# Performance work log

Measured on AMD Instinct MI355X. Metric: run time of the kernel, lower is better.

Reference implementation:

```python
import jax, jax.numpy as jnp
import numpy as np

B, S, D = 4, 8192, 1024
H = 16
HD = D // H          # 64
AD = 64              # approx_dim
EPS = 1e-6


def setup_inputs() -> dict:
    key = jax.random.key(0)
    ks = jax.random.split(key, 5)
    x = jax.random.normal(ks[0], (B, S, D), dtype=jnp.float32)
    # qkv_proj: Linear(D, 3*D)
    W_qkv = jax.random.normal(ks[1], (3 * D, D), dtype=jnp.float32) * (1.0 / np.sqrt(D))
    b_qkv = jnp.zeros((3 * D,), dtype=jnp.float32)
    # proj: Linear(HD, AD) with xavier_uniform init, zero bias
    limit = np.sqrt(6.0 / (HD + AD))
    W_p = jax.random.uniform(ks[2], (AD, HD), dtype=jnp.float32, minval=-limit, maxval=limit)
    b_p = jnp.zeros((AD,), dtype=jnp.float32)
    return {"x": x, "W_qkv": W_qkv, "b_qkv": b_qkv, "W_p": W_p, "b_p": b_p}


def reference(x, W_qkv, b_qkv, W_p, b_p):
    # qkv projection and split
    qkv = x @ W_qkv.T + b_qkv                      # [B,S,3D]
    Q, K, V = jnp.split(qkv, 3, axis=-1)
    # [B,S,D] -> [B,H,S,HD]
    def to_heads(t):
        return t.reshape(B, S, H, HD).transpose(0, 2, 1, 3)
    Q, K, V = to_heads(Q), to_heads(K), to_heads(V)
    # shared projection to approx dim, feature map phi(u) = sqrt(1 + u^2)
    pQ = jnp.einsum('bhsd,ad->bhsa', Q, W_p) + b_p
    pK = jnp.einsum('bhsd,ad->bhsa', K, W_p) + b_p
    phi_Q = jnp.sqrt(1.0 + pQ * pQ)                # [B,H,S,AD]
    phi_K = jnp.sqrt(1.0 + pK * pK)
    # linear attention: O(S) chained contractions
    KTV = jnp.einsum('bhsa,bhsv->bhav', phi_K, V)  # [B,H,AD,HD]
    numerator = jnp.einsum('bhsa,bhav->bhsv', phi_Q, KTV)  # [B,H,S,HD]
    k_sum = phi_K.sum(axis=2)                      # [B,H,AD]
    denominator = jnp.einsum('bhsa,bha->bhs', phi_Q, k_sum)  # [B,H,S]
    head_out = numerator / (denominator[..., None] + EPS)
    # [B,H,S,HD] -> [B,S,D]
    return head_out.transpose(0, 2, 1, 3).reshape(B, S, D)
```

## Files before the change

### kernel.cpp

```cpp
#include <hip/hip_runtime.h>
#include <hip/hip_bf16.h>
#include <cstdint>

static constexpr int Bc  = 4;
static constexpr int Sc  = 8192;
static constexpr int Dc  = 1024;
static constexpr int Hc  = 16;
static constexpr int BHc = Bc * Hc;
static constexpr int Mc  = Bc * Sc;
static constexpr int N3c = 3 * Dc;
static constexpr float EPSc = 1e-6f;

using bf16x8 = __attribute__((ext_vector_type(8))) __bf16;
using f32x4  = __attribute__((ext_vector_type(4))) float;

__device__ __forceinline__ ushort f2bf(float f) {
  union { float f; uint32_t u; } v; v.f = f;
  uint32_t u = v.u;
  return (ushort)((u + 0x7fffu + ((u >> 16) & 1u)) >> 16);
}
__device__ __forceinline__ float bf2f(ushort h) {
  union { uint32_t u; float f; } v; v.u = ((uint32_t)h) << 16;
  return v.f;
}

typedef const __attribute__((address_space(1))) unsigned int* gas_u32p;
typedef __attribute__((address_space(3))) unsigned int* las_u32p;
__device__ __forceinline__ void gld_lds16(const void* g, void* l) {
  __builtin_amdgcn_global_load_lds((gas_u32p)g, (las_u32p)l, 16, 0, 0);
}

__global__ __launch_bounds__(256) void cvt_bf16_k(const float* __restrict__ src,
                                                  ushort* __restrict__ dst, int n4) {
  for (int i = blockIdx.x * 256 + threadIdx.x; i < n4; i += gridDim.x * 256) {
    float4 v = reinterpret_cast<const float4*>(src)[i];
    ushort4 o; o.x = f2bf(v.x); o.y = f2bf(v.y); o.z = f2bf(v.z); o.w = f2bf(v.w);
    reinterpret_cast<ushort4*>(dst)[i] = o;
  }
}

__global__ __launch_bounds__(256) void fold_k(const float* __restrict__ Wq,
                                              const float* __restrict__ Wp,
                                              const float* __restrict__ bq,
                                              const float* __restrict__ bp,
                                              ushort* __restrict__ W3b,
                                              float* __restrict__ bias3) {
  const int bx = blockIdx.x;
  const int p = bx >> 4, h = bx & 15;
  const int t = threadIdx.x;
  if (p == 2) {
    const int base = 2048 + h * 64;
    for (int li = t; li < 64 * 256; li += 256) {
      int r = li >> 8, c4 = (li & 255) * 4;
      float4 v = *reinterpret_cast<const float4*>(&Wq[(size_t)(base + r) * 1024 + c4]);
      ushort4 o; o.x = f2bf(v.x); o.y = f2bf(v.y); o.z = f2bf(v.z); o.w = f2bf(v.w);
      *reinterpret_cast<ushort4*>(&W3b[(size_t)(base + r) * 1024 + c4]) = o;
    }
    if (t < 64) bias3[base + t] = bq[base + t];
    return;
  }
  __shared__ ushort Ws[64 * 64];
  __shared__ ushort Tq[256 * 64];
  const int rbase = p * 1024 + h * 64;
  for (int li = t; li < 64 * 16; li += 256) {
    int a = li >> 4, h4 = (li & 15) * 4;
    float4 v = *reinterpret_cast<const float4*>(&Wp[a * 64 + h4]);
    ushort4 o; o.x = f2bf(v.x); o.y = f2bf(v.y); o.z = f2bf(v.z); o.w = f2bf(v.w);
    *reinterpret_cast<ushort4*>(&Ws[a * 64 + h4]) = o;
  }
  if (t < 64) {
    float s = bp[t];
    for (int hd = 0; hd < 64; ++hd) s += Wp[t * 64 + hd] * bq[rbase + hd];
    bias3[rbase + t] = s;
  }
  const int w = t >> 6, lane = t & 63, lr = lane & 15, kg = lane >> 4;
  for (int dt = 0; dt < 4; ++dt) {
    __syncthreads();
    for (int li = t; li < 64 * 64; li += 256) {
      int hd = li >> 6, d4 = (li & 63) * 4;
      float4 v = *reinterpret_cast<const float4*>(&Wq[(size_t)(rbase + hd) * 1024 + dt * 256 + d4]);
      Tq[(d4 + 0) * 64 + hd] = f2bf(v.x);
      Tq[(d4 + 1) * 64 + hd] = f2bf(v.y);
      Tq[(d4 + 2) * 64 + hd] = f2bf(v.z);
      Tq[(d4 + 3) * 64 + hd] = f2bf(v.w);
    }
    __syncthreads();
    f32x4 acc[4][4];
#pragma unroll
    for (int i = 0; i < 4; i++)
#pragma unroll
      for (int j = 0; j < 4; j++) acc[i][j] = (f32x4){0.f, 0.f, 0.f, 0.f};
#pragma unroll
    for (int kk = 0; kk < 2; ++kk) {
      bf16x8 af[4], bfr[4];
#pragma unroll
      for (int i = 0; i < 4; i++)
        af[i] = *reinterpret_cast<const bf16x8*>(&Ws[(i * 16 + lr) * 64 + kk * 32 + kg * 8]);
#pragma unroll
      for (int j = 0; j < 4; j++)
        bfr[j] = *reinterpret_cast<const bf16x8*>(&Tq[(w * 64 + j * 16 + lr) * 64 + kk * 32 + kg * 8]);
#pragma unroll
      for (int i = 0; i < 4; i++)
#pragma unroll
        for (int j = 0; j < 4; j++)
          acc[i][j] = __builtin_amdgcn_mfma_f32_16x16x32_bf16(af[i], bfr[j], acc[i][j], 0, 0, 0);
    }
#pragma unroll
    for (int i = 0; i < 4; i++)
#pragma unroll
      for (int j = 0; j < 4; j++)
#pragma unroll
        for (int r = 0; r < 4; r++)
          W3b[(size_t)(rbase + i * 16 + kg * 4 + r) * 1024 + dt * 256 + w * 64 + j * 16 + lr] =
              f2bf(acc[i][j][r]);
  }
}

__global__ __launch_bounds__(512, 2) void gemm_pipe_k(const ushort* __restrict__ xb,
                                                      const ushort* __restrict__ W3b,
                                                      const float* __restrict__ bias3,
                                                      ushort* __restrict__ Qb,
                                                      ushort* __restrict__ KTb,
                                                      ushort* __restrict__ VTb) {
  __shared__ __align__(16) ushort As[4 * 8192];
  __shared__ __align__(16) ushort Bs[4 * 8192];
  const int t = threadIdx.x, wave = t >> 6, lane = t & 63;
  const int lr = lane & 15, kg = lane >> 4;
  const int wr = wave >> 2, wc = wave & 3;

  const int flat = blockIdx.x;
  const int swz  = (flat & 7) * 192 + (flat >> 3);
  const int n0 = (swz % 12) * 256;
  const int m0 = (swz / 12) * 256;

  const int srow = t >> 2;
  const int sg   = (t & 3) ^ ((t >> 3) & 3);
  const int swb  = wave * 512;

  auto STAGE = [&](int tile, int buf) {
    const int kt = tile * 32;
#pragma unroll
    for (int is = 0; is < 2; ++is) {
      gld_lds16(xb  + (size_t)(m0 + is * 128 + srow) * 1024 + kt + sg * 8,
                As + buf * 8192 + is * 4096 + swb);
      gld_lds16(W3b + (size_t)(n0 + is * 128 + srow) * 1024 + kt + sg * 8,
                Bs + buf * 8192 + is * 4096 + swb);
    }
  };

  f32x4 acc[8][4];
#pragma unroll
  for (int f = 0; f < 8; f++)
#pragma unroll
    for (int j = 0; j < 4; j++) acc[f][j] = (f32x4){0.f, 0.f, 0.f, 0.f};

  const int cp = (kg ^ ((lr >> 1) & 3)) * 8;
  const ushort* Ard = As + (wr * 128 + lr) * 32 + cp;
  const ushort* Brd = Bs + (wc * 64 + lr) * 32 + cp;

  auto COMPUTE = [&](int buf) {
    bf16x8 af[8], bfr[4];
    const ushort* Ab = Ard + buf * 8192;
    const ushort* Bb = Brd + buf * 8192;
#pragma unroll
    for (int f = 0; f < 8; f++) af[f] = *reinterpret_cast<const bf16x8*>(Ab + f * 512);
#pragma unroll
    for (int j = 0; j < 4; j++) bfr[j] = *reinterpret_cast<const bf16x8*>(Bb + j * 512);
    __builtin_amdgcn_s_setprio(1);
#pragma unroll
    for (int f = 0; f < 8; f++)
#pragma unroll
      for (int j = 0; j < 4; j++)
        acc[f][j] = __builtin_amdgcn_mfma_f32_16x16x32_bf16(af[f], bfr[j], acc[f][j], 0, 0, 0);
    __builtin_amdgcn_s_setprio(0);
  };

  STAGE(0, 0);
  STAGE(1, 1);
  STAGE(2, 2);
  asm volatile("s_waitcnt vmcnt(8)" ::: "memory");
  __builtin_amdgcn_s_barrier();

#pragma unroll 1
  for (int i = 0; i < 7; ++i) {
    const int tb = i * 4;
#pragma unroll
    for (int j = 0; j < 4; ++j) {
      STAGE(tb + j + 3, (j + 3) & 3);
      COMPUTE(j);
      asm volatile("s_waitcnt vmcnt(8)" ::: "memory");
      __builtin_amdgcn_s_barrier();
    }
  }
  STAGE(31, 3);
  COMPUTE(0);
  asm volatile("s_waitcnt vmcnt(8)" ::: "memory");
  __builtin_amdgcn_s_barrier();
  COMPUTE(1);
  asm volatile("s_waitcnt vmcnt(4)" ::: "memory");
  __builtin_amdgcn_s_barrier();
  COMPUTE(2);
  asm volatile("s_waitcnt vmcnt(0)" ::: "memory");
  __builtin_amdgcn_s_barrier();
  COMPUTE(3);

  const int n0w  = n0 + wc * 64;
  const int part = n0w >> 10;
  const int h    = (n0w & 1023) >> 6;
  const int bq   = m0 >> 13;
  const int s_base = (m0 & 8191) + wr * 128;
  float bias[4];
#pragma unroll
  for (int j = 0; j < 4; j++) bias[j] = bias3[n0w + j * 16 + lr];

  if (part == 0) {
    ushort* dst = Qb + ((size_t)(bq * Hc + h)) * Sc * 64;
#pragma unroll
    for (int f = 0; f < 8; f++)
#pragma unroll
      for (int j = 0; j < 4; j++)
#pragma unroll
        for (int r = 0; r < 4; r++) {
          float p = acc[f][j][r] + bias[j];
          dst[(size_t)(s_base + f * 16 + kg * 4 + r) * 64 + j * 16 + lr] =
              f2bf(sqrtf(1.f + p * p));
        }
  } else {
    ushort* dst = ((part == 1) ? KTb : VTb) + ((size_t)(bq * Hc + h)) * 64 * Sc;
#pragma unroll
    for (int f = 0; f < 8; f++) {
      const int s = s_base + f * 16 + kg * 4;
#pragma unroll
      for (int j = 0; j < 4; j++) {
        ushort4 o;
        if (part == 1) {
#pragma unroll
          for (int r = 0; r < 4; r++) {
            float p = acc[f][j][r] + bias[j];
            (&o.x)[r] = f2bf(sqrtf(1.f + p * p));
          }
        } else {
#pragma unroll
          for (int r = 0; r < 4; r++) (&o.x)[r] = f2bf(acc[f][j][r] + bias[j]);
        }
        *reinterpret_cast<ushort4*>(&dst[(size_t)(j * 16 + lr) * Sc + s]) = o;
      }
    }
  }
}

__global__ __launch_bounds__(256) void ktv_part_k(const ushort* __restrict__ KT,
                                                  const ushort* __restrict__ VT,
                                                  float* __restrict__ KTVp,
                                                  float* __restrict__ ksump) {
  __shared__ __align__(16) ushort Ks[64 * 128];
  __shared__ __align__(16) ushort Vs[64 * 128];
  __shared__ float red[64][65];
  const int t = threadIdx.x, chunk = blockIdx.x, bh = blockIdx.y;
  const int wave = t >> 6, lane = t & 63, lr = lane & 15, kg = lane >> 4;
  const size_t hb = (size_t)bh * 64 * Sc;
  const int s0 = chunk * 1024;

  f32x4 acc[4][4];
#pragma unroll
  for (int i = 0; i < 4; i++)
#pragma unroll
    for (int j = 0; j < 4; j++) acc[i][j] = (f32x4){0.f, 0.f, 0.f, 0.f};
  float ks_acc = 0.f;

  const int srl = t >> 4;
  const int scc = (t & 15) ^ ((t >> 4) & 7);
  const int wb  = (t >> 6) * 512;
  const int cR = ((wave * 4 + kg) ^ (lr & 7)) * 8;

  for (int st = 0; st < 8; ++st) {
    const int sb = s0 + st * 128;
    __syncthreads();
#pragma unroll
    for (int is = 0; is < 4; ++is) {
      const int row = is * 16 + srl;
      gld_lds16(KT + hb + (size_t)row * Sc + sb + scc * 8, Ks + is * 2048 + wb);
      gld_lds16(VT + hb + (size_t)row * Sc + sb + scc * 8, Vs + is * 2048 + wb);
    }
    __syncthreads();
    {
      bf16x8 af[4], bfr[4];
#pragma unroll
      for (int i = 0; i < 4; i++)
        af[i] = *reinterpret_cast<const bf16x8*>(&Ks[(i * 16 + lr) * 128 + cR]);
#pragma unroll
      for (int j = 0; j < 4; j++)
        bfr[j] = *reinterpret_cast<const bf16x8*>(&Vs[(j * 16 + lr) * 128 + cR]);
#pragma unroll
      for (int i = 0; i < 4; i++)
#pragma unroll
        for (int j = 0; j < 4; j++)
          acc[i][j] = __builtin_amdgcn_mfma_f32_16x16x32_bf16(af[i], bfr[j], acc[i][j], 0, 0, 0);
    }
    if (t < 64) {
      float s = 0.f;
      for (int e = 0; e < 128; e++) s += bf2f(Ks[t * 128 + e]);
      ks_acc += s;
    }
  }

  __syncthreads();
  for (int li = t; li < 64 * 65; li += 256) (&red[0][0])[li] = 0.f;
  __syncthreads();
  for (int w = 0; w < 4; w++) {
    if (wave == w) {
#pragma unroll
      for (int i = 0; i < 4; i++)
#pragma unroll
        for (int j = 0; j < 4; j++)
#pragma unroll
          for (int r = 0; r < 4; r++)
            red[i * 16 + kg * 4 + r][j * 16 + lr] += acc[i][j][r];
    }
    __syncthreads();
  }
  float* outp = KTVp + ((size_t)bh * 8 + chunk) * 4096;
  for (int li = t; li < 4096; li += 256) outp[li] = red[li >> 6][li & 63];
  if (t < 64) ksump[((size_t)bh * 8 + chunk) * 64 + t] = ks_acc;
}

__global__ __launch_bounds__(256) void ktv_red_k(const float* __restrict__ KTVp,
                                                 const float* __restrict__ ksump,
                                                 float* __restrict__ KTV,
                                                 float* __restrict__ ksum) {
  const int bh = blockIdx.x, t = threadIdx.x;
  for (int li = t; li < 4096; li += 256) {
    float s = 0.f;
    for (int c = 0; c < 8; c++) s += KTVp[((size_t)bh * 8 + c) * 4096 + li];
    KTV[(size_t)bh * 4096 + li] = s;
  }
  if (t < 64) {
    float s = 0.f;
    for (int c = 0; c < 8; c++) s += ksump[((size_t)bh * 8 + c) * 64 + t];
    ksum[bh * 64 + t] = s;
  }
}

__global__ __launch_bounds__(256) void out_k(const ushort* __restrict__ Qphi,
                                             const float* __restrict__ KTV,
                                             const float* __restrict__ ksum,
                                             float* __restrict__ out) {
  __shared__ ushort Qs[256][72];
  __shared__ ushort BT[64][72];
  __shared__ float  den[256];
  __shared__ float  kss[64];
  const int t = threadIdx.x;
  const int bh = blockIdx.y, s0 = blockIdx.x * 256;
  const ushort* qb = Qphi + (size_t)bh * Sc * 64 + (size_t)s0 * 64;

#pragma unroll
  for (int i = 0; i < 8; i++) {
    int li = i * 256 + t;
    int r = li >> 3, c8 = li & 7;
    *reinterpret_cast<uint4*>(&Qs[r][c8 * 8]) = *reinterpret_cast<const uint4*>(&qb[li * 8]);
  }
  for (int li = t; li < 4096; li += 256) {
    int a = li >> 6, v = li & 63;
    BT[v][a] = f2bf(KTV[(size_t)bh * 4096 + li]);
  }
  if (t < 64) kss[t] = ksum[bh * 64 + t];
  __syncthreads();

  {
    float d = 0.f;
    for (int a = 0; a < 64; a++) d += bf2f(Qs[t][a]) * kss[a];
    den[t] = d + EPSc;
  }
  __syncthreads();

  const int wave = t >> 6, lane = t & 63, lr = lane & 15, kg = lane >> 4;
  f32x4 acc[4][4];
#pragma unroll
  for (int i = 0; i < 4; i++)
#pragma unroll
    for (int j = 0; j < 4; j++) acc[i][j] = (f32x4){0.f, 0.f, 0.f, 0.f};

#pragma unroll
  for (int ks = 0; ks < 64; ks += 32) {
    bf16x8 af[4], bfr[4];
#pragma unroll
    for (int i = 0; i < 4; i++)
      af[i] = *reinterpret_cast<const bf16x8*>(&Qs[wave * 64 + i * 16 + lr][ks + kg * 8]);
#pragma unroll
    for (int j = 0; j < 4; j++)
      bfr[j] = *reinterpret_cast<const bf16x8*>(&BT[j * 16 + lr][ks + kg * 8]);
#pragma unroll
    for (int i = 0; i < 4; i++)
#pragma unroll
      for (int j = 0; j < 4; j++)
        acc[i][j] = __builtin_amdgcn_mfma_f32_16x16x32_bf16(af[i], bfr[j], acc[i][j], 0, 0, 0);
  }

  const int bq = bh >> 4, h = bh & 15;
#pragma unroll
  for (int i = 0; i < 4; i++) {
#pragma unroll
    for (int j = 0; j < 4; j++) {
#pragma unroll
      for (int r = 0; r < 4; r++) {
        int row = wave * 64 + i * 16 + kg * 4 + r;
        int s = s0 + row;
        int v = j * 16 + lr;
        out[((size_t)bq * Sc + s) * 1024 + h * 64 + v] = acc[i][j][r] / den[row];
      }
    }
  }
}

extern "C" void kernel_launch(void* const* d_in, const int* in_sizes, int n_in,
                              void* d_out, int out_size, void* d_ws, size_t ws_size,
                              hipStream_t stream) {
  const float* x     = (const float*)d_in[0];
  const float* W_qkv = (const float*)d_in[1];
  const float* b_qkv = (const float*)d_in[2];
  const float* W_p   = (const float*)d_in[3];
  const float* b_p   = (const float*)d_in[4];
  float* out = (float*)d_out;

  size_t off = 0;
  auto carve = [&](size_t bytes) -> void* {
    void* p = (char*)d_ws + off;
    off += (bytes + 255) & ~(size_t)255;
    return p;
  };
  const size_t headElems = (size_t)BHc * Sc * 64;
  ushort* xb    = (ushort*)carve((size_t)Mc * Dc * 2);
  ushort* Qb    = (ushort*)carve(headElems * 2);
  ushort* KTb   = (ushort*)carve(headElems * 2);
  ushort* VTb   = (ushort*)carve(headElems * 2);
  ushort* W3b   = (ushort*)carve((size_t)N3c * Dc * 2);
  float*  bias3 = (float*)carve((size_t)N3c * 4);
  float*  KTVp  = (float*)carve((size_t)BHc * 8 * 4096 * 4);
  float*  ksmp  = (float*)carve((size_t)BHc * 8 * 64 * 4);
  float*  KTV   = (float*)carve((size_t)BHc * 4096 * 4);
  float*  ksum  = (float*)carve((size_t)BHc * 64 * 4);
  (void)ws_size; (void)n_in; (void)in_sizes; (void)out_size;

  cvt_bf16_k<<<2048, 256, 0, stream>>>(x, xb, Mc * Dc / 4);
  fold_k<<<48, 256, 0, stream>>>(W_qkv, W_p, b_qkv, b_p, W3b, bias3);
  gemm_pipe_k<<<(Mc / 256) * (N3c / 256), 512, 0, stream>>>(xb, W3b, bias3, Qb, KTb, VTb);
  ktv_part_k<<<dim3(8, BHc), 256, 0, stream>>>(KTb, VTb, KTVp, ksmp);
  ktv_red_k<<<BHc, 256, 0, stream>>>(KTVp, ksmp, KTV, ksum);
  out_k<<<dim3(Sc / 256, BHc), 256, 0, stream>>>(Qb, KTV, ksum, out);
}
```

Before: 417.5 us.

## Restructure QKV GEMM mainloop into 64-wide K double buffer with interleaved staging

Result: slower. 441.1 us (+5.7%).

```diff
diff --git a/kernel.cpp b/kernel.cpp
--- a/kernel.cpp
+++ b/kernel.cpp
@@ -29,6 +29,9 @@
 __device__ __forceinline__ void gld_lds16(const void* g, void* l) {
   __builtin_amdgcn_global_load_lds((gas_u32p)g, (las_u32p)l, 16, 0, 0);
 }
+
+#define FENCE asm volatile("" ::: "memory")
+#define BARF  do { FENCE; __builtin_amdgcn_s_barrier(); FENCE; } while (0)
 
 __global__ __launch_bounds__(256) void cvt_bf16_k(const float* __restrict__ src,
                                                   ushort* __restrict__ dst, int n4) {
@@ -122,8 +125,8 @@
                                                       ushort* __restrict__ Qb,
                                                       ushort* __restrict__ KTb,
                                                       ushort* __restrict__ VTb) {
-  __shared__ __align__(16) ushort As[4 * 8192];
-  __shared__ __align__(16) ushort Bs[4 * 8192];
+  __shared__ __align__(16) ushort As[2 * 16384];
+  __shared__ __align__(16) ushort Bs[2 * 16384];
   const int t = threadIdx.x, wave = t >> 6, lane = t & 63;
   const int lr = lane & 15, kg = lane >> 4;
   const int wr = wave >> 2, wc = wave & 3;
@@ -133,19 +136,23 @@
   const int n0 = (swz % 12) * 256;
   const int m0 = (swz / 12) * 256;
 
-  const int srow = t >> 2;
-  const int sg   = (t & 3) ^ ((t >> 3) & 3);
-  const int swb  = wave * 512;
-
-  auto STAGE = [&](int tile, int buf) {
-    const int kt = tile * 32;
-#pragma unroll
-    for (int is = 0; is < 2; ++is) {
-      gld_lds16(xb  + (size_t)(m0 + is * 128 + srow) * 1024 + kt + sg * 8,
-                As + buf * 8192 + is * 4096 + swb);
-      gld_lds16(W3b + (size_t)(n0 + is * 128 + srow) * 1024 + kt + sg * 8,
-                Bs + buf * 8192 + is * 4096 + swb);
-    }
+  const int srow8 = wave * 8 + (lane >> 3);
+  const int sg    = (lane & 7) ^ (lane >> 3);
+  const int swb   = wave * 512;
+
+  auto stageA = [&](int tile, int buf, int h) {
+    const int col = tile * 64 + sg * 8;
+#pragma unroll
+    for (int i2 = 0; i2 < 2; ++i2)
+      gld_lds16(xb + (size_t)(m0 + h * 128 + i2 * 64 + srow8) * 1024 + col,
+                As + buf * 16384 + h * 8192 + i2 * 4096 + swb);
+  };
+  auto stageB = [&](int tile, int buf, int h) {
+    const int col = tile * 64 + sg * 8;
+#pragma unroll
+    for (int i2 = 0; i2 < 2; ++i2)
+      gld_lds16(W3b + (size_t)(n0 + h * 128 + i2 * 64 + srow8) * 1024 + col,
+                Bs + buf * 16384 + h * 8192 + i2 * 4096 + swb);
   };
 
   f32x4 acc[8][4];
@@ -154,55 +161,72 @@
 #pragma unroll
     for (int j = 0; j < 4; j++) acc[f][j] = (f32x4){0.f, 0.f, 0.f, 0.f};
 
-  const int cp = (kg ^ ((lr >> 1) & 3)) * 8;
-  const ushort* Ard = As + (wr * 128 + lr) * 32 + cp;
-  const ushort* Brd = Bs + (wc * 64 + lr) * 32 + cp;
-
-  auto COMPUTE = [&](int buf) {
-    bf16x8 af[8], bfr[4];
-    const ushort* Ab = Ard + buf * 8192;
-    const ushort* Bb = Brd + buf * 8192;
-#pragma unroll
-    for (int f = 0; f < 8; f++) af[f] = *reinterpret_cast<const bf16x8*>(Ab + f * 512);
-#pragma unroll
-    for (int j = 0; j < 4; j++) bfr[j] = *reinterpret_cast<const bf16x8*>(Bb + j * 512);
+  auto readA4 = [&](int buf, int fh, int kk, bf16x8* a) {
+#pragma unroll
+    for (int f = 0; f < 4; f++) {
+      const int row = wr * 128 + fh * 64 + f * 16 + lr;
+      const int gp  = (kk * 4 + kg) ^ (lr & 7);
+      a[f] = *reinterpret_cast<const bf16x8*>(As + buf * 16384 + row * 64 + gp * 8);
+    }
+  };
+  auto readB4 = [&](int buf, int kk, bf16x8* b) {
+#pragma unroll
+    for (int j = 0; j < 4; j++) {
+      const int row = wc * 64 + j * 16 + lr;
+      const int gp  = (kk * 4 + kg) ^ (lr & 7);
+      b[j] = *reinterpret_cast<const bf16x8*>(Bs + buf * 16384 + row * 64 + gp * 8);
+    }
+  };
+  auto mfma16 = [&](const bf16x8* a, const bf16x8* b, int fh) {
     __builtin_amdgcn_s_setprio(1);
 #pragma unroll
-    for (int f = 0; f < 8; f++)
-#pragma unroll
-      for (int j = 0; j < 4; j++)
-        acc[f][j] = __builtin_amdgcn_mfma_f32_16x16x32_bf16(af[f], bfr[j], acc[f][j], 0, 0, 0);
+    for (int f = 0; f < 4; f++)
+#pragma unroll
+      for (int j = 0; j < 4; j++)
+        acc[fh * 4 + f][j] =
+            __builtin_amdgcn_mfma_f32_16x16x32_bf16(a[f], b[j], acc[fh * 4 + f][j], 0, 0, 0);
     __builtin_amdgcn_s_setprio(0);
   };
 
-  STAGE(0, 0);
-  STAGE(1, 1);
-  STAGE(2, 2);
-  asm volatile("s_waitcnt vmcnt(8)" ::: "memory");
-  __builtin_amdgcn_s_barrier();
+  stageB(0, 0, 0); stageB(0, 0, 1);
+  stageA(0, 0, 0); stageA(0, 0, 1);
+  stageB(1, 1, 0); stageB(1, 1, 1);
+  asm volatile("s_waitcnt vmcnt(4)" ::: "memory");
+  BARF;
+
+  bf16x8 a[4], b[4];
+  auto TILE = [&](int T, int buf, bool stA, bool stB, int W) {
+    if (stA) stageA(T + 1, buf ^ 1, 0);
+    readB4(buf, 0, b);
+    readA4(buf, 0, 0, a);
+    BARF;
+    mfma16(a, b, 0);
+    BARF;
+    if (stA) stageA(T + 1, buf ^ 1, 1);
+    readA4(buf, 1, 0, a);
+    BARF;
+    mfma16(a, b, 1);
+    BARF;
+    readB4(buf, 1, b);
+    readA4(buf, 0, 1, a);
+    BARF;
+    mfma16(a, b, 0);
+    BARF;
+    if (stB) { stageB(T + 2, buf, 0); stageB(T + 2, buf, 1); }
+    readA4(buf, 1, 1, a);
+    BARF;
+    mfma16(a, b, 1);
+    if (W == 4) asm volatile("s_waitcnt vmcnt(4)" ::: "memory");
+    else        asm volatile("s_waitcnt vmcnt(0)" ::: "memory");
+    BARF;
+  };
 
 #pragma unroll 1
-  for (int i = 0; i < 7; ++i) {
-    const int tb = i * 4;
-#pragma unroll
-    for (int j = 0; j < 4; ++j) {
-      STAGE(tb + j + 3, (j + 3) & 3);
-      COMPUTE(j);
-      asm volatile("s_waitcnt vmcnt(8)" ::: "memory");
-      __builtin_amdgcn_s_barrier();
-    }
-  }
-  STAGE(31, 3);
-  COMPUTE(0);
-  asm volatile("s_waitcnt vmcnt(8)" ::: "memory");
-  __builtin_amdgcn_s_barrier();
-  COMPUTE(1);
-  asm volatile("s_waitcnt vmcnt(4)" ::: "memory");
-  __builtin_amdgcn_s_barrier();
-  COMPUTE(2);
-  asm volatile("s_waitcnt vmcnt(0)" ::: "memory");
-  __builtin_amdgcn_s_barrier();
-  COMPUTE(3);
+  for (int tt = 0; tt < 8; ++tt) {
+    const int T0 = tt * 2, T1 = T0 + 1;
+    TILE(T0, 0, true,     T0 < 14, (T0 <= 13) ? 4 : 0);
+    TILE(T1, 1, T1 < 15,  T1 < 14, (T1 <= 13) ? 4 : 0);
+  }
 
   const int n0w  = n0 + wc * 64;
   const int part = n0w >> 10;
```

## Load B operand directly from global into registers, dropping its LDS staging

Applied to the files above, without the earlier changes.

Result: slower. 495.2 us (+18.6%).

```diff
diff --git a/kernel.cpp b/kernel.cpp
--- a/kernel.cpp
+++ b/kernel.cpp
@@ -123,29 +123,32 @@
                                                       ushort* __restrict__ KTb,
                                                       ushort* __restrict__ VTb) {
   __shared__ __align__(16) ushort As[4 * 8192];
-  __shared__ __align__(16) ushort Bs[4 * 8192];
   const int t = threadIdx.x, wave = t >> 6, lane = t & 63;
   const int lr = lane & 15, kg = lane >> 4;
   const int wr = wave >> 2, wc = wave & 3;
 
   const int flat = blockIdx.x;
-  const int swz  = (flat & 7) * 192 + (flat >> 3);
-  const int n0 = (swz % 12) * 256;
-  const int m0 = (swz / 12) * 256;
+  const int xcd = flat & 7, idx = flat >> 3;
+  const int m0 = ((xcd >> 1) * 32 + idx / 6) * 256;
+  const int n0 = ((xcd & 1) * 6 + idx % 6) * 256;
 
   const int srow = t >> 2;
   const int sg   = (t & 3) ^ ((t >> 3) & 3);
   const int swb  = wave * 512;
 
-  auto STAGE = [&](int tile, int buf) {
-    const int kt = tile * 32;
-#pragma unroll
-    for (int is = 0; is < 2; ++is) {
-      gld_lds16(xb  + (size_t)(m0 + is * 128 + srow) * 1024 + kt + sg * 8,
+  auto stageA = [&](int tile, int buf) {
+#pragma unroll
+    for (int is = 0; is < 2; ++is)
+      gld_lds16(xb + (size_t)(m0 + is * 128 + srow) * 1024 + tile * 32 + sg * 8,
                 As + buf * 8192 + is * 4096 + swb);
-      gld_lds16(W3b + (size_t)(n0 + is * 128 + srow) * 1024 + kt + sg * 8,
-                Bs + buf * 8192 + is * 4096 + swb);
-    }
+  };
+
+  const int n0w = n0 + wc * 64;
+  auto loadB = [&](int tile, bf16x8 (&bb)[4]) {
+#pragma unroll
+    for (int j = 0; j < 4; ++j)
+      bb[j] = *reinterpret_cast<const bf16x8*>(
+          W3b + (size_t)(n0w + j * 16 + lr) * 1024 + tile * 32 + kg * 8);
   };
 
   f32x4 acc[8][4];
@@ -156,55 +159,71 @@
 
   const int cp = (kg ^ ((lr >> 1) & 3)) * 8;
   const ushort* Ard = As + (wr * 128 + lr) * 32 + cp;
-  const ushort* Brd = Bs + (wc * 64 + lr) * 32 + cp;
-
-  auto COMPUTE = [&](int buf) {
-    bf16x8 af[8], bfr[4];
+
+  auto compute = [&](int buf, const bf16x8 (&bb)[4]) {
     const ushort* Ab = Ard + buf * 8192;
-    const ushort* Bb = Brd + buf * 8192;
-#pragma unroll
-    for (int f = 0; f < 8; f++) af[f] = *reinterpret_cast<const bf16x8*>(Ab + f * 512);
-#pragma unroll
-    for (int j = 0; j < 4; j++) bfr[j] = *reinterpret_cast<const bf16x8*>(Bb + j * 512);
+    bf16x8 a[4];
+#pragma unroll
+    for (int f = 0; f < 4; ++f) a[f] = *reinterpret_cast<const bf16x8*>(Ab + f * 512);
     __builtin_amdgcn_s_setprio(1);
 #pragma unroll
-    for (int f = 0; f < 8; f++)
-#pragma unroll
-      for (int j = 0; j < 4; j++)
-        acc[f][j] = __builtin_amdgcn_mfma_f32_16x16x32_bf16(af[f], bfr[j], acc[f][j], 0, 0, 0);
+    for (int f = 0; f < 4; ++f)
+#pragma unroll
+      for (int j = 0; j < 4; ++j)
+        acc[f][j] = __builtin_amdgcn_mfma_f32_16x16x32_bf16(a[f], bb[j], acc[f][j], 0, 0, 0);
+    __builtin_amdgcn_s_setprio(0);
+#pragma unroll
+    for (int f = 0; f < 4; ++f) a[f] = *reinterpret_cast<const bf16x8*>(Ab + (f + 4) * 512);
+    __builtin_amdgcn_s_setprio(1);
+#pragma unroll
+    for (int f = 0; f < 4; ++f)
+#pragma unroll
+      for (int j = 0; j < 4; ++j)
+        acc[f + 4][j] = __builtin_amdgcn_mfma_f32_16x16x32_bf16(a[f], bb[j], acc[f + 4][j], 0, 0, 0);
     __builtin_amdgcn_s_setprio(0);
   };
 
-  STAGE(0, 0);
-  STAGE(1, 1);
-  STAGE(2, 2);
-  asm volatile("s_waitcnt vmcnt(8)" ::: "memory");
-  __builtin_amdgcn_s_barrier();
-
-#pragma unroll 1
-  for (int i = 0; i < 7; ++i) {
-    const int tb = i * 4;
-#pragma unroll
-    for (int j = 0; j < 4; ++j) {
-      STAGE(tb + j + 3, (j + 3) & 3);
-      COMPUTE(j);
-      asm volatile("s_waitcnt vmcnt(8)" ::: "memory");
-      __builtin_amdgcn_s_barrier();
-    }
-  }
-  STAGE(31, 3);
-  COMPUTE(0);
-  asm volatile("s_waitcnt vmcnt(8)" ::: "memory");
-  __builtin_amdgcn_s_barrier();
-  COMPUTE(1);
-  asm volatile("s_waitcnt vmcnt(4)" ::: "memory");
-  __builtin_amdgcn_s_barrier();
-  COMPUTE(2);
+  bf16x8 b0[4], b1[4];
+  stageA(0, 0); stageA(1, 1); stageA(2, 2);
+  loadB(0, b0);
   asm volatile("s_waitcnt vmcnt(0)" ::: "memory");
   __builtin_amdgcn_s_barrier();
-  COMPUTE(3);
-
-  const int n0w  = n0 + wc * 64;
+
+#pragma unroll 1
+  for (int tt = 0; tt < 14; ++tt) {
+    const int t0 = tt * 2;
+    stageA(t0 + 3, (t0 + 3) & 3);
+    loadB(t0 + 1, b1);
+    asm volatile("s_waitcnt vmcnt(6)" ::: "memory");
+    compute(t0 & 3, b0);
+    asm volatile("" ::: "memory");
+    __builtin_amdgcn_s_barrier();
+    stageA(t0 + 4, (t0 + 4) & 3);
+    loadB(t0 + 2, b0);
+    asm volatile("s_waitcnt vmcnt(6)" ::: "memory");
+    compute((t0 + 1) & 3, b1);
+    asm volatile("" ::: "memory");
+    __builtin_amdgcn_s_barrier();
+  }
+  stageA(31, 3);
+  loadB(29, b1);
+  asm volatile("s_waitcnt vmcnt(6)" ::: "memory");
+  compute(0, b0);
+  asm volatile("" ::: "memory");
+  __builtin_amdgcn_s_barrier();
+  loadB(30, b0);
+  asm volatile("s_waitcnt vmcnt(4)" ::: "memory");
+  compute(1, b1);
+  asm volatile("" ::: "memory");
+  __builtin_amdgcn_s_barrier();
+  loadB(31, b1);
+  asm volatile("s_waitcnt vmcnt(4)" ::: "memory");
+  compute(2, b0);
+  asm volatile("" ::: "memory");
+  __builtin_amdgcn_s_barrier();
+  asm volatile("s_waitcnt vmcnt(0)" ::: "memory");
+  compute(3, b1);
+
   const int part = n0w >> 10;
   const int h    = (n0w & 1023) >> 6;
   const int bq   = m0 >> 13;
```

## Double-buffer KTV partial kernel, split output rows across waves, MFMA key sum

Applied to the files above, without the earlier changes.

Result: faster. 408.3 us (-2.2%).

```diff
diff --git a/kernel.cpp b/kernel.cpp
--- a/kernel.cpp
+++ b/kernel.cpp
@@ -249,79 +249,77 @@
   }
 }
 
-__global__ __launch_bounds__(256) void ktv_part_k(const ushort* __restrict__ KT,
-                                                  const ushort* __restrict__ VT,
-                                                  float* __restrict__ KTVp,
-                                                  float* __restrict__ ksump) {
-  __shared__ __align__(16) ushort Ks[64 * 128];
-  __shared__ __align__(16) ushort Vs[64 * 128];
-  __shared__ float red[64][65];
+__global__ __launch_bounds__(256, 2) void ktv_part_k(const ushort* __restrict__ KT,
+                                                     const ushort* __restrict__ VT,
+                                                     float* __restrict__ KTVp,
+                                                     float* __restrict__ ksump) {
+  __shared__ __align__(16) ushort Ks[2 * 8192];
+  __shared__ __align__(16) ushort Vs[2 * 8192];
   const int t = threadIdx.x, chunk = blockIdx.x, bh = blockIdx.y;
   const int wave = t >> 6, lane = t & 63, lr = lane & 15, kg = lane >> 4;
   const size_t hb = (size_t)bh * 64 * Sc;
   const int s0 = chunk * 1024;
 
-  f32x4 acc[4][4];
-#pragma unroll
-  for (int i = 0; i < 4; i++)
-#pragma unroll
-    for (int j = 0; j < 4; j++) acc[i][j] = (f32x4){0.f, 0.f, 0.f, 0.f};
-  float ks_acc = 0.f;
+  f32x4 acc[4];
+  f32x4 acc_ks;
+#pragma unroll
+  for (int j = 0; j < 4; j++) acc[j] = (f32x4){0.f, 0.f, 0.f, 0.f};
+  acc_ks = (f32x4){0.f, 0.f, 0.f, 0.f};
+
+  bf16x8 ones;
+#pragma unroll
+  for (int e = 0; e < 8; e++) ones[e] = (__bf16)1.0f;
 
   const int srl = t >> 4;
   const int scc = (t & 15) ^ ((t >> 4) & 7);
   const int wb  = (t >> 6) * 512;
-  const int cR = ((wave * 4 + kg) ^ (lr & 7)) * 8;
-
-  for (int st = 0; st < 8; ++st) {
+
+  auto STG = [&](int st, int buf) {
     const int sb = s0 + st * 128;
-    __syncthreads();
 #pragma unroll
     for (int is = 0; is < 4; ++is) {
       const int row = is * 16 + srl;
-      gld_lds16(KT + hb + (size_t)row * Sc + sb + scc * 8, Ks + is * 2048 + wb);
-      gld_lds16(VT + hb + (size_t)row * Sc + sb + scc * 8, Vs + is * 2048 + wb);
-    }
+      gld_lds16(KT + hb + (size_t)row * Sc + sb + scc * 8, Ks + buf * 8192 + is * 2048 + wb);
+      gld_lds16(VT + hb + (size_t)row * Sc + sb + scc * 8, Vs + buf * 8192 + is * 2048 + wb);
+    }
+  };
+
+  auto COMPUTE = [&](int buf) {
+    const ushort* Kb = Ks + buf * 8192;
+    const ushort* Vb = Vs + buf * 8192;
+#pragma unroll
+    for (int ks4 = 0; ks4 < 4; ++ks4) {
+      const int pos = ((ks4 * 4 + kg) ^ (lr & 7)) * 8;
+      bf16x8 af = *reinterpret_cast<const bf16x8*>(Kb + (wave * 16 + lr) * 128 + pos);
+      acc_ks = __builtin_amdgcn_mfma_f32_16x16x32_bf16(af, ones, acc_ks, 0, 0, 0);
+#pragma unroll
+      for (int j = 0; j < 4; ++j) {
+        bf16x8 bv = *reinterpret_cast<const bf16x8*>(Vb + (j * 16 + lr) * 128 + pos);
+        acc[j] = __builtin_amdgcn_mfma_f32_16x16x32_bf16(af, bv, acc[j], 0, 0, 0);
+      }
+    }
+  };
+
+  STG(0, 0);
+  __syncthreads();
+#pragma unroll 1
+  for (int st = 0; st < 8; ++st) {
+    if (st < 7) STG(st + 1, (st + 1) & 1);
+    COMPUTE(st & 1);
     __syncthreads();
-    {
-      bf16x8 af[4], bfr[4];
-#pragma unroll
-      for (int i = 0; i < 4; i++)
-        af[i] = *reinterpret_cast<const bf16x8*>(&Ks[(i * 16 + lr) * 128 + cR]);
-#pragma unroll
-      for (int j = 0; j < 4; j++)
-        bfr[j] = *reinterpret_cast<const bf16x8*>(&Vs[(j * 16 + lr) * 128 + cR]);
-#pragma unroll
-      for (int i = 0; i < 4; i++)
-#pragma unroll
-        for (int j = 0; j < 4; j++)
-          acc[i][j] = __builtin_amdgcn_mfma_f32_16x16x32_bf16(af[i], bfr[j], acc[i][j], 0, 0, 0);
-    }
-    if (t < 64) {
-      float s = 0.f;
-      for (int e = 0; e < 128; e++) s += bf2f(Ks[t * 128 + e]);
-      ks_acc += s;
-    }
-  }
-
-  __syncthreads();
-  for (int li = t; li < 64 * 65; li += 256) (&red[0][0])[li] = 0.f;
-  __syncthreads();
-  for (int w = 0; w < 4; w++) {
-    if (wave == w) {
-#pragma unroll
-      for (int i = 0; i < 4; i++)
-#pragma unroll
-        for (int j = 0; j < 4; j++)
-#pragma unroll
-          for (int r = 0; r < 4; r++)
-            red[i * 16 + kg * 4 + r][j * 16 + lr] += acc[i][j][r];
-    }
-    __syncthreads();
-  }
+  }
+
   float* outp = KTVp + ((size_t)bh * 8 + chunk) * 4096;
-  for (int li = t; li < 4096; li += 256) outp[li] = red[li >> 6][li & 63];
-  if (t < 64) ksump[((size_t)bh * 8 + chunk) * 64 + t] = ks_acc;
+#pragma unroll
+  for (int j = 0; j < 4; ++j)
+#pragma unroll
+    for (int r = 0; r < 4; ++r)
+      outp[(wave * 16 + kg * 4 + r) * 64 + j * 16 + lr] = acc[j][r];
+  if (lr == 0) {
+#pragma unroll
+    for (int r = 0; r < 4; ++r)
+      ksump[((size_t)bh * 8 + chunk) * 64 + wave * 16 + kg * 4 + r] = acc_ks[r];
+  }
 }
 
 __global__ __launch_bounds__(256) void ktv_red_k(const float* __restrict__ KTVp,
```
